# Kernel optimization log

Measured on AMD Instinct MI355X. Metric: run time of the kernel, lower is better.

The kernel has to match this reference:

```python
import math
import jax, jax.numpy as jnp
import numpy as np


def _precompute_psi(nlat_in, nlon_in, nlat_out, K, theta_cutoff):
    """Faithful numpy port of _precompute_convolution_tensor (equiangular grids).
    Returns COO indices (k, t, lat_in, lon_in) and float values of the sparse
    filter tensor psi of logical shape [K, nlat_out, nlat_in*nlon_in]."""
    lats_in = np.linspace(0.0, np.pi, nlat_in)
    lats_out = np.linspace(0.0, np.pi, nlat_out)
    phis = np.linspace(-np.pi, np.pi, nlon_in)
    d_theta = theta_cutoff / K
    theta_i = np.arange(K) * d_theta  # (K,)
    ks, ts, las, los, vs = [], [], [], [], []
    alpha = -lats_in[:, None]          # (nlat_in, 1)
    beta = phis[None, :]               # (1, nlon_in)
    for t in range(nlat_out):
        gamma = lats_out[t]
        z = np.cos(alpha) * np.cos(gamma) - np.cos(beta) * np.sin(alpha) * np.sin(gamma)
        theta = np.arccos(np.clip(z, -1.0, 1.0))   # (nlat_in, nlon_in)
        diff = np.abs(theta[None, :, :] - theta_i[:, None, None])  # (K, nlat_in, nlon_in)
        mask = (diff < d_theta) & (theta[None, :, :] < theta_cutoff)
        k_idx, la_idx, lo_idx = np.nonzero(mask)
        v = 1.0 - diff[k_idx, la_idx, lo_idx] / d_theta  # triangle (hat) weights
        ks.append(k_idx); ts.append(np.full_like(k_idx, t)); las.append(la_idx); los.append(lo_idx); vs.append(v)
    return (np.concatenate(ks).astype(np.int32),
            np.concatenate(ts).astype(np.int32),
            np.concatenate(las).astype(np.int32),
            np.concatenate(los).astype(np.int32),
            np.concatenate(vs).astype(np.float32))


def setup_inputs() -> dict:
    B, C = 4, 32
    nlat_in, nlon_in = 361, 720
    nlat_out, nlon_out = 361, 720
    K = 3
    theta_cutoff = 0.01 * math.pi  # default used at the precompute call site
    k, t, la, lo, v = _precompute_psi(nlat_in, nlon_in, nlat_out, K, theta_cutoff)
    key = jax.random.key(0)
    x = jax.random.normal(key, (B, C, nlat_in, nlon_in), dtype=jnp.float32)
    return {
        "x": x,
        "psi_vals": jnp.asarray(v),
        "psi_k": jnp.asarray(k),
        "psi_t": jnp.asarray(t),
        "psi_lat": jnp.asarray(la),
        "psi_lon": jnp.asarray(lo),
        "kernel_size": K,
        "nlat_out": nlat_out,
        "nlon_out": nlon_out,
    }


def reference(x, psi_vals, psi_k, psi_t, psi_lat, psi_lon, kernel_size, nlat_out, nlon_out):
    B, C, nlat_in, nlon_in = x.shape
    BC = B * C
    scale = nlon_in // nlon_out  # = 1 here
    # (nlat_in, nlon_in, BC) layout, matching x.reshape(B*C,...).permute(1,2,0)
    xr = x.reshape(BC, nlat_in, nlon_in).transpose(1, 2, 0)
    seg = psi_k * nlat_out + psi_t           # row id in the (K*nlat_out) output
    num_seg = kernel_size * nlat_out

    def step(_, p):
        # torch.roll(x, scale, dims=lon) applied (p+1) times before the bmm:
        # rolled[lat, lon] = x[lat, (lon - (p+1)*scale) % nlon]
        lon_idx = (psi_lon - (p + 1) * scale) % nlon_in
        g = xr[psi_lat, lon_idx]             # (nnz, BC) irregular gather
        out_p = jax.ops.segment_sum(psi_vals[:, None] * g, seg, num_segments=num_seg)
        return None, out_p                   # (K*nlat_out, BC)

    _, outs = jax.lax.scan(step, None, jnp.arange(nlon_out))  # (nlon_out, K*nlat_out, BC)
    outs = outs.reshape(nlon_out, kernel_size, nlat_out, BC)
    # permute(3,1,2,0) then split BC -> (B, C)
    return outs.transpose(3, 1, 2, 0).reshape(B, C, kernel_size, nlat_out, nlon_out)
```

## Files before the change

### kernel.cpp

```cpp
#include <hip/hip_runtime.h>
#include <math.h>


#define NLAT 361
#define NLON 720
#define KK 3
#define PTILE 48
#define NPX 15
#define NT 384
#define PD 56
#define SWN 832
#define TOTCAP (720*1024)

typedef __attribute__((ext_vector_type(8))) short bf16x8;
typedef __attribute__((ext_vector_type(4))) float f32x4;
typedef __attribute__((ext_vector_type(4))) unsigned int u32x4;

#define D_PI 3.14159265358979311599796346854418516159057617187500
#define STEP_LAT (D_PI / 360.0)
#define STEP_PHI ((2.0 * D_PI) / 719.0)
#define CUTOFF (0.01 * D_PI)
#define DTH (CUTOFF / 3.0)

__device__ __forceinline__ void gll16(const void* g, void* l) {
    __builtin_amdgcn_global_load_lds(
        (const __attribute__((address_space(1))) void*)g,
        (__attribute__((address_space(3))) void*)l, 16, 0, 0);
}
__device__ __forceinline__ void gll4(const void* g, void* l) {
    __builtin_amdgcn_global_load_lds(
        (const __attribute__((address_space(1))) void*)g,
        (__attribute__((address_space(3))) void*)l, 4, 0, 0);
}

__device__ inline unsigned int bf16pair_rne(float lo, float hi) {
    unsigned int a = __builtin_bit_cast(unsigned int, lo);
    unsigned int b = __builtin_bit_cast(unsigned int, hi);
    a = a + 0x7fffu + ((a >> 16) & 1u);
    b = b + 0x7fffu + ((b >> 16) & 1u);
    return (a >> 16) | (b & 0xffff0000u);
}

__global__ __launch_bounds__(512) void bounds_kernel(int4* __restrict__ params,
                                                     float2* __restrict__ pAB,
                                                     unsigned long long* __restrict__ actd) {
    __shared__ int part[512];
    int tid = threadIdx.x;
    int rmins[9], Ws[9], bl8s[9];
    float As[9], Bs[9];
    int wsum = 0;
    if (tid < NLAT) {
        int t = tid;
        double g = (t == 360) ? D_PI : (double)t * STEP_LAT;
        double cg = cos(g), sg = sin(g);
        const double coscut = cos(CUTOFF);
#pragma unroll
        for (int d = 0; d < 9; ++d) {
            int la = t + d - 4;
            int rmin = 0, W = 0;
            double A = 0.0, Bc = 0.0;
            if (la >= 0 && la <= 360) {
                double lad = (la == 360) ? D_PI : (double)la * STEP_LAT;
                A = cos(lad) * cg;
                Bc = sin(lad) * sg;
                if (Bc < 1e-14) {
                    if (A > coscut) { rmin = 0; W = 720; }
                } else {
                    double C = (coscut - A) / Bc;
                    if (C <= -1.0) { rmin = 0; W = 720; }
                    else if (C < 1.0) {
                        double bmax = acos(C);
                        int r0 = (int)floor((D_PI - bmax) / STEP_PHI) + 1;
                        int r1 = (int)ceil((D_PI + bmax) / STEP_PHI) - 1;
                        if (r0 < 0) r0 = 0;
                        if (r1 > 719) r1 = 719;
                        rmin = r0; W = r1 - r0 + 1;
                        if (W < 0) W = 0;
                    }
                }
            }
            rmins[d] = rmin; Ws[d] = W;
            As[d] = (float)A; Bs[d] = (float)Bc;
            int b8 = 0;
            if (W > 0) {
                b8 = (W + 111) & ~7;
                if (b8 > SWN) b8 = SWN;
            }
            bl8s[d] = b8;
            wsum += b8;
        }
    }
    part[tid] = wsum;
    __syncthreads();
    for (int dd = 1; dd < 512; dd <<= 1) {
        int v = part[tid];
        int w2 = (tid >= dd) ? part[tid - dd] : 0;
        __syncthreads();
        part[tid] = v + w2;
        __syncthreads();
    }
    int base = part[tid] - wsum;
    if (tid < NLAT) {
        unsigned long long pk = 0;
        int nact = 0;
#pragma unroll
        for (int d = 0; d < 9; ++d) {
            int off = base;
            base += bl8s[d];
            if (Ws[d] > 0 && off + bl8s[d] <= TOTCAP) {
                params[tid * 9 + d] = make_int4(rmins[d], Ws[d], off, bl8s[d]);
                pAB[tid * 9 + d] = make_float2(As[d], Bs[d]);
                pk |= ((unsigned long long)d) << (4 + 4 * nact);
                nact++;
            } else {
                params[tid * 9 + d] = make_int4(0, 0, 0, 0);
            }
        }
        pk |= (unsigned long long)nact;
        actd[tid] = pk;
    }
}

__global__ __launch_bounds__(256) void fill_cvt_kernel(const int4* __restrict__ params,
                                                       const float2* __restrict__ pAB,
                                                       unsigned int* __restrict__ wtab,
                                                       const float* __restrict__ x,
                                                       unsigned int* __restrict__ xb,
                                                       int n8, int do_cvt) {
    int bid = blockIdx.x;
    if (bid < NLAT * 9) {
        int4 pr = params[bid];
        int W = pr.y;
        if (W <= 0) return;
        int rmin = pr.x, off = pr.z, bl8 = pr.w;
        float2 ab = pAB[bid];
        float A = ab.x, Bc = ab.y;
        const float invd = (float)(1.0 / DTH);
        for (int idx = threadIdx.x; idx < bl8; idx += 256) {
            int j = idx - PD;
            float f1 = 1.0e9f, f2 = 1.0e9f;
            if (j >= 0 && j < W) {
                int lo = rmin + j;
                float beta = (lo == 719) ? (float)D_PI : (float)((double)lo * STEP_PHI - D_PI);
                float z = fminf(1.f, fmaxf(-1.f, fmaf(Bc, cosf(beta), A)));
                f1 = acosf(z) * invd;
            }
            if (j + 1 >= 0 && j + 1 < W) {
                int lo = rmin + j + 1;
                float beta = (lo == 719) ? (float)D_PI : (float)((double)lo * STEP_PHI - D_PI);
                float z = fminf(1.f, fmaxf(-1.f, fmaf(Bc, cosf(beta), A)));
                f2 = acosf(z) * invd;
            }
            float w0a = fmaxf(0.f, 1.f - f1);
            float w1a = fmaxf(0.f, 1.f - fabsf(f1 - 1.f));
            float w2a = fmaxf(0.f, 1.f - fabsf(f1 - 2.f));
            float w0b = fmaxf(0.f, 1.f - f2);
            float w1b = fmaxf(0.f, 1.f - fabsf(f2 - 1.f));
            float w2b = fmaxf(0.f, 1.f - fabsf(f2 - 2.f));
            wtab[0 * TOTCAP + off + idx] = bf16pair_rne(w0a, w0b);
            wtab[1 * TOTCAP + off + idx] = bf16pair_rne(w1a, w1b);
            wtab[2 * TOTCAP + off + idx] = bf16pair_rne(w2a, w2b);
        }
    } else if (do_cvt) {
        int cb = bid - NLAT * 9;
        for (int i = cb * 256 + threadIdx.x; i < n8; i += 2048 * 256) {
            f32x4 a = *(const f32x4*)(x + (size_t)i * 8);
            f32x4 b = *(const f32x4*)(x + (size_t)i * 8 + 4);
            u32x4 q;
            q.x = bf16pair_rne(a.x, a.y);
            q.y = bf16pair_rne(a.z, a.w);
            q.z = bf16pair_rne(b.x, b.y);
            q.w = bf16pair_rne(b.z, b.w);
            *(u32x4*)(xb + (size_t)i * 4) = q;
        }
    }
}

template <int USEBF16>
__global__ __launch_bounds__(NT, 4) void dconv_mfma_kernel(
    const float* __restrict__ x, const unsigned short* __restrict__ xb,
    const int4* __restrict__ params, const unsigned long long* __restrict__ actd,
    const unsigned int* __restrict__ wtab, float* __restrict__ out) {
    __shared__ __attribute__((aligned(16))) unsigned char sB[2][128 * 128];
    __shared__ unsigned int sWi[2][KK * SWN];

    int bid = blockIdx.x;
    int r = bid & 7;
    int rest = bid >> 3;
    int px = rest % NPX;
    int q = rest / NPX;
    int yp = 8 * q + r;
    if (yp > 360) return;
    int t = (yp & 1) ? (360 - (yp >> 1)) : (yp >> 1);
    int p0 = px * PTILE;
    int tid = threadIdx.x;
    int lane = tid & 63;
    int w = tid >> 6;
    int psub = w >> 1;
    int bc0w = (w & 1) * 64;
    int l15 = lane & 15;
    int l4 = lane >> 4;

    f32x4 acc[4][KK];
#pragma unroll
    for (int n = 0; n < 4; ++n)
#pragma unroll
        for (int k = 0; k < KK; ++k) acc[n][k] = (f32x4){0.f, 0.f, 0.f, 0.f};

    unsigned long long pk = actd[t];
    int nact = (int)(pk & 15ull);

    int c = 0, iact = 0;
    int la = 0, W = 0, off = 0, bl8 = 0, mbase = 0, shift = 0;
    int nK = 0, nC = 1, ks_lo = 0, ks_hi = -1;

    auto LOADP = [&](int dd) {
        la = t + dd - 4;
        int4 pr = params[t * 9 + dd];
        int rmin = pr.x;
        W = pr.y; off = pr.z; bl8 = pr.w;
        int ms0 = rmin - 48 - p0;
        shift = (ms0 + 720) & 7;
        nK = (W + 47 + shift + 31) >> 5;
        nC = (nK + 1) >> 1;
        mbase = (((ms0 - shift) % 720) + 720) % 720;
        int s_off = psub * 16 + 9 - shift;
        int kl = (9 - s_off + 31) >> 5;
        ks_lo = kl < 0 ? 0 : kl;
        int kh = (55 + W - s_off) >> 5;
        ks_hi = kh > nK - 1 ? nK - 1 : kh;
    };

    auto ISSUE = [&](int cc, bool rowstart, int pbuf, int rbuf) {
#pragma unroll
        for (int pass = 0; pass < 3; ++pass) {
            int slot = pass * NT + tid;
            if (slot < 1024) {
                int bc = slot >> 3;
                int g = slot & 7;
                int gs = g ^ (bc & 7);
                int mg = mbase + cc * 64 + gs * 8;
                mg -= (mg >= 720) ? 720 : 0;
                mg -= (mg >= 720) ? 720 : 0;
                mg -= (mg >= 720) ? 720 : 0;
                if (USEBF16) {
                    gll16(xb + ((size_t)bc * NLAT + la) * NLON + mg,
                          &sB[pbuf][slot * 16]);
                } else {
                    const float* src = x + ((size_t)bc * NLAT + la) * NLON + mg;
                    f32x4 a = *(const f32x4*)(src);
                    f32x4 b = *(const f32x4*)(src + 4);
                    u32x4 qq;
                    qq.x = bf16pair_rne(a.x, a.y);
                    qq.y = bf16pair_rne(a.z, a.w);
                    qq.z = bf16pair_rne(b.x, b.y);
                    qq.w = bf16pair_rne(b.z, b.w);
                    *(u32x4*)(&sB[pbuf][slot * 16]) = qq;
                }
            }
        }
        if (rowstart) {
#pragma unroll
            for (int pass = 0; pass < 3; ++pass) {
                int idx = pass * NT + tid;
                if (idx < bl8) {
                    if (USEBF16) {
                        gll4(wtab + 0 * TOTCAP + off + idx, &sWi[rbuf][0 * SWN + idx]);
                        gll4(wtab + 1 * TOTCAP + off + idx, &sWi[rbuf][1 * SWN + idx]);
                        gll4(wtab + 2 * TOTCAP + off + idx, &sWi[rbuf][2 * SWN + idx]);
                    } else {
                        sWi[rbuf][0 * SWN + idx] = wtab[0 * TOTCAP + off + idx];
                        sWi[rbuf][1 * SWN + idx] = wtab[1 * TOTCAP + off + idx];
                        sWi[rbuf][2 * SWN + idx] = wtab[2 * TOTCAP + off + idx];
                    }
                }
            }
        }
    };

    LOADP((int)((pk >> 4) & 15ull));
    ISSUE(0, true, 0, 0);
    int pb = 0, rw = 0;

    while (true) {
        int shiftS = shift;
        int c2 = c * 2;
        int kloS = ks_lo > c2 ? ks_lo : c2;
        int khiS = ks_hi < c2 + 1 ? ks_hi : c2 + 1;
        int pbC = pb, rwC = rw;
        bool done = false, nrow = false;
        if (c + 1 < nC) {
            c = c + 1;
        } else if (iact + 1 < nact) {
            iact++;
            c = 0;
            LOADP((int)((pk >> (4 + 4 * iact)) & 15ull));
            nrow = true;
        } else {
            done = true;
        }
        if (USEBF16) asm volatile("s_waitcnt vmcnt(0)" ::: "memory");
        __syncthreads();
        if (!done) {
            pb ^= 1;
            if (nrow) rw ^= 1;
            ISSUE(c, nrow, pb, rw);
        }
        __builtin_amdgcn_s_setprio(1);
        int soffS = psub * 16 + 9 - shiftS;
        for (int ks = kloS; ks <= khiS; ++ks) {
            int ksl = ks - c2;
            int s = ks * 32 + l4 * 8 + soffS + l15;
            bf16x8 af[KK];
#pragma unroll
            for (int k = 0; k < KK; ++k) {
                const unsigned int* wp = &sWi[rwC][k * SWN + s];
                u32x4 qf;
                qf.x = wp[0];
                qf.y = wp[2];
                qf.z = wp[4];
                qf.w = wp[6];
                af[k] = __builtin_bit_cast(bf16x8, qf);
            }
            int colbase = ksl * 64 + l4 * 16;
#pragma unroll
            for (int n = 0; n < 4; ++n) {
                int brow = bc0w + n * 16 + l15;
                int colb = colbase ^ ((brow & 7) << 4);
                bf16x8 bfv = *(const bf16x8*)(&sB[pbC][brow * 128 + colb]);
                acc[n][0] = __builtin_amdgcn_mfma_f32_16x16x32_bf16(af[0], bfv, acc[n][0], 0, 0, 0);
                acc[n][1] = __builtin_amdgcn_mfma_f32_16x16x32_bf16(af[1], bfv, acc[n][1], 0, 0, 0);
                acc[n][2] = __builtin_amdgcn_mfma_f32_16x16x32_bf16(af[2], bfv, acc[n][2], 0, 0, 0);
            }
        }
        __builtin_amdgcn_s_setprio(0);
        if (done) break;
    }

    int p = p0 + psub * 16 + l4 * 4;
#pragma unroll
    for (int n = 0; n < 4; ++n) {
        int bc = bc0w + n * 16 + l15;
#pragma unroll
        for (int k = 0; k < KK; ++k) {
            float* o = out + (((size_t)bc * KK + k) * NLAT + t) * NLON + p;
            *(f32x4*)o = acc[n][k];
        }
    }
}

extern "C" void kernel_launch(void* const* d_in, const int* in_sizes, int n_in,
                              void* d_out, int out_size, void* d_ws, size_t ws_size,
                              hipStream_t stream) {
    const float* x = (const float*)d_in[0];
    float* out = (float*)d_out;

    char* ws = (char*)d_ws;
    int4* params = (int4*)(ws + 0);
    float2* pAB = (float2*)(ws + 53248);
    unsigned long long* actd = (unsigned long long*)(ws + 81920);
    unsigned int* wtab = (unsigned int*)(ws + 90112);
    size_t xb_off = (90112 + (size_t)3 * TOTCAP * 4 + 4095) & ~(size_t)4095;
    size_t xb_bytes = (size_t)128 * NLAT * NLON * 2;
    int use_bf16 = (ws_size >= xb_off + xb_bytes) ? 1 : 0;
    unsigned short* xb = (unsigned short*)(ws + xb_off);

    int n8 = 128 * NLAT * NLON / 8;

    bounds_kernel<<<1, 512, 0, stream>>>(params, pAB, actd);
    fill_cvt_kernel<<<NLAT * 9 + 2048, 256, 0, stream>>>(params, pAB, wtab, x,
                                                         (unsigned int*)xb, n8, use_bf16);

    dim3 grid(8 * NPX * 46, 1, 1);
    if (use_bf16) {
        dconv_mfma_kernel<1><<<grid, NT, 0, stream>>>(x, xb, params, actd, wtab, out);
    } else {
        dconv_mfma_kernel<0><<<grid, NT, 0, stream>>>(x, xb, params, actd, wtab, out);
    }
}
```

Before: 287.6 us.

## Repack weight window per chunk into contiguous quads for vector LDS reads

```diff
diff --git a/kernel.cpp b/kernel.cpp
--- a/kernel.cpp
+++ b/kernel.cpp
@@ -10,6 +10,7 @@
 #define NT 384
 #define PD 56
 #define SWN 832
+#define SWNP_Q 128
 #define TOTCAP (720*1024)
 
 typedef __attribute__((ext_vector_type(8))) short bf16x8;
@@ -182,7 +183,7 @@
     const int4* __restrict__ params, const unsigned long long* __restrict__ actd,
     const unsigned int* __restrict__ wtab, float* __restrict__ out) {
     __shared__ __attribute__((aligned(16))) unsigned char sB[2][128 * 128];
-    __shared__ unsigned int sWi[2][KK * SWN];
+    __shared__ __attribute__((aligned(16))) unsigned int sWi[2][KK * SWNP_Q * 4];
 
     int bid = blockIdx.x;
     int r = bid & 7;
@@ -231,7 +232,7 @@
         ks_hi = kh > nK - 1 ? nK - 1 : kh;
     };
 
-    auto ISSUE = [&](int cc, bool rowstart, int pbuf, int rbuf) {
+    auto ISSUE = [&](int cc, int pbuf) {
 #pragma unroll
         for (int pass = 0; pass < 3; ++pass) {
             int slot = pass * NT + tid;
@@ -259,43 +260,43 @@
                 }
             }
         }
-        if (rowstart) {
-#pragma unroll
-            for (int pass = 0; pass < 3; ++pass) {
-                int idx = pass * NT + tid;
-                if (idx < bl8) {
-                    if (USEBF16) {
-                        gll4(wtab + 0 * TOTCAP + off + idx, &sWi[rbuf][0 * SWN + idx]);
-                        gll4(wtab + 1 * TOTCAP + off + idx, &sWi[rbuf][1 * SWN + idx]);
-                        gll4(wtab + 2 * TOTCAP + off + idx, &sWi[rbuf][2 * SWN + idx]);
-                    } else {
-                        sWi[rbuf][0 * SWN + idx] = wtab[0 * TOTCAP + off + idx];
-                        sWi[rbuf][1 * SWN + idx] = wtab[1 * TOTCAP + off + idx];
-                        sWi[rbuf][2 * SWN + idx] = wtab[2 * TOTCAP + off + idx];
-                    }
+        int W0 = cc * 64 + 9 - shift;
+        int gmax = off + bl8 - 1;
+#pragma unroll
+        for (int pass = 0; pass < 4; ++pass) {
+            int i = pass * NT + tid;
+            if (i < KK * SWNP_Q * 4) {
+                int plane = i >> 9;
+                int rem = i & 511;
+                int e = rem >> 2;
+                int qq = rem & 3;
+                int gidx = off + W0 + e + 2 * qq;
+                gidx = (gidx > gmax) ? gmax : gidx;
+                if (USEBF16) {
+                    gll4(wtab + (size_t)plane * TOTCAP + gidx, &sWi[pbuf][i]);
+                } else {
+                    sWi[pbuf][i] = wtab[(size_t)plane * TOTCAP + gidx];
                 }
             }
         }
     };
 
     LOADP((int)((pk >> 4) & 15ull));
-    ISSUE(0, true, 0, 0);
-    int pb = 0, rw = 0;
+    ISSUE(0, 0);
+    int pb = 0;
 
     while (true) {
-        int shiftS = shift;
         int c2 = c * 2;
         int kloS = ks_lo > c2 ? ks_lo : c2;
         int khiS = ks_hi < c2 + 1 ? ks_hi : c2 + 1;
-        int pbC = pb, rwC = rw;
-        bool done = false, nrow = false;
+        int pbC = pb;
+        bool done = false;
         if (c + 1 < nC) {
             c = c + 1;
         } else if (iact + 1 < nact) {
             iact++;
             c = 0;
             LOADP((int)((pk >> (4 + 4 * iact)) & 15ull));
-            nrow = true;
         } else {
             done = true;
         }
@@ -303,24 +304,16 @@
         __syncthreads();
         if (!done) {
             pb ^= 1;
-            if (nrow) rw ^= 1;
-            ISSUE(c, nrow, pb, rw);
+            ISSUE(c, pb);
         }
         __builtin_amdgcn_s_setprio(1);
-        int soffS = psub * 16 + 9 - shiftS;
         for (int ks = kloS; ks <= khiS; ++ks) {
             int ksl = ks - c2;
-            int s = ks * 32 + l4 * 8 + soffS + l15;
+            int e = ksl * 32 + l4 * 8 + psub * 16 + l15;
             bf16x8 af[KK];
 #pragma unroll
             for (int k = 0; k < KK; ++k) {
-                const unsigned int* wp = &sWi[rwC][k * SWN + s];
-                u32x4 qf;
-                qf.x = wp[0];
-                qf.y = wp[2];
-                qf.z = wp[4];
-                qf.w = wp[6];
-                af[k] = __builtin_bit_cast(bf16x8, qf);
+                af[k] = *(const bf16x8*)(&sWi[pbC][(k * SWNP_Q + e) * 4]);
             }
             int colbase = ksl * 64 + l4 * 16;
 #pragma unroll
```

After: 308.0 us. 7.1% more time.

## Split wide latitude rows into sub-row segments to shrink weight LDS buffer

Applied to the files above, without the earlier changes.

```diff
diff --git a/kernel.cpp b/kernel.cpp
--- a/kernel.cpp
+++ b/kernel.cpp
@@ -10,7 +10,8 @@
 #define NT 384
 #define PD 56
 #define SWN 832
-#define TOTCAP (720*1024)
+#define SWNL 336
+#define TOTCAP (576*1024)
 
 typedef __attribute__((ext_vector_type(8))) short bf16x8;
 typedef __attribute__((ext_vector_type(4))) float f32x4;
@@ -43,7 +44,8 @@
 
 __global__ __launch_bounds__(512) void bounds_kernel(int4* __restrict__ params,
                                                      float2* __restrict__ pAB,
-                                                     unsigned long long* __restrict__ actd) {
+                                                     unsigned long long* __restrict__ actd,
+                                                     int4* __restrict__ pex) {
     __shared__ int part[512];
     int tid = threadIdx.x;
     int rmins[9], Ws[9], bl8s[9];
@@ -101,8 +103,7 @@
     }
     int base = part[tid] - wsum;
     if (tid < NLAT) {
-        unsigned long long pk = 0;
-        int nact = 0;
+        int cnt = 0;
 #pragma unroll
         for (int d = 0; d < 9; ++d) {
             int off = base;
@@ -110,14 +111,20 @@
             if (Ws[d] > 0 && off + bl8s[d] <= TOTCAP) {
                 params[tid * 9 + d] = make_int4(rmins[d], Ws[d], off, bl8s[d]);
                 pAB[tid * 9 + d] = make_float2(As[d], Bs[d]);
-                pk |= ((unsigned long long)d) << (4 + 4 * nact);
-                nact++;
+                int la = tid + d - 4;
+                int nKmax = (Ws[d] + 85) >> 5;
+                for (int a = 0; a < nKmax; a += 8) {
+                    if (cnt < 32) {
+                        pex[tid * 32 + cnt] =
+                            make_int4(la | (a << 16), Ws[d], rmins[d], off);
+                        cnt++;
+                    }
+                }
             } else {
                 params[tid * 9 + d] = make_int4(0, 0, 0, 0);
             }
         }
-        pk |= (unsigned long long)nact;
-        actd[tid] = pk;
+        actd[tid] = (unsigned long long)cnt;
     }
 }
 
@@ -179,10 +186,10 @@
 template <int USEBF16>
 __global__ __launch_bounds__(NT, 4) void dconv_mfma_kernel(
     const float* __restrict__ x, const unsigned short* __restrict__ xb,
-    const int4* __restrict__ params, const unsigned long long* __restrict__ actd,
+    const int4* __restrict__ pex, const unsigned long long* __restrict__ actd,
     const unsigned int* __restrict__ wtab, float* __restrict__ out) {
     __shared__ __attribute__((aligned(16))) unsigned char sB[2][128 * 128];
-    __shared__ unsigned int sWi[2][KK * SWN];
+    __shared__ unsigned int sWi[2][KK * SWNL];
 
     int bid = blockIdx.x;
     int r = bid & 7;
@@ -207,28 +214,42 @@
 #pragma unroll
         for (int k = 0; k < KK; ++k) acc[n][k] = (f32x4){0.f, 0.f, 0.f, 0.f};
 
-    unsigned long long pk = actd[t];
-    int nact = (int)(pk & 15ull);
+    int nact = (int)actd[t];
 
     int c = 0, iact = 0;
-    int la = 0, W = 0, off = 0, bl8 = 0, mbase = 0, shift = 0;
-    int nK = 0, nC = 1, ks_lo = 0, ks_hi = -1;
-
-    auto LOADP = [&](int dd) {
-        la = t + dd - 4;
-        int4 pr = params[t * 9 + dd];
-        int rmin = pr.x;
-        W = pr.y; off = pr.z; bl8 = pr.w;
+    int la = 0, W = 0, offsub = 0, gmax = 0, mbase = 0, shift = 0, asub = 0;
+    int nC = 1, ks_lo = 0, ks_hi = -1;
+
+    auto LOADP = [&](int i) {
+        int4 pr = pex[t * 32 + i];
+        la = pr.x & 0xFFFF;
+        asub = pr.x >> 16;
+        W = pr.y;
+        int rmin = pr.z;
+        int offrow = pr.w;
         int ms0 = rmin - 48 - p0;
         shift = (ms0 + 720) & 7;
-        nK = (W + 47 + shift + 31) >> 5;
-        nC = (nK + 1) >> 1;
-        mbase = (((ms0 - shift) % 720) + 720) % 720;
+        int nKg = (W + 47 + shift + 31) >> 5;
+        int mb = (((ms0 - shift) % 720) + 720) % 720;
+        mbase = mb + asub * 32;
+        mbase -= (mbase >= 720) ? 720 : 0;
+        mbase -= (mbase >= 720) ? 720 : 0;
+        offsub = offrow + asub * 32;
+        int bl8 = (W + 111) & ~7;
+        if (bl8 > SWN) bl8 = SWN;
+        gmax = offrow + bl8 - 1;
+        int nKp = nKg - asub;
+        if (nKp > 8) nKp = 8;
+        nC = (nKp <= 0) ? 1 : ((nKp + 1) >> 1);
         int s_off = psub * 16 + 9 - shift;
         int kl = (9 - s_off + 31) >> 5;
-        ks_lo = kl < 0 ? 0 : kl;
+        if (kl < 0) kl = 0;
+        if (kl < asub) kl = asub;
+        ks_lo = kl;
         int kh = (55 + W - s_off) >> 5;
-        ks_hi = kh > nK - 1 ? nK - 1 : kh;
+        if (kh > nKg - 1) kh = nKg - 1;
+        if (kh > asub + nKp - 1) kh = asub + nKp - 1;
+        ks_hi = kh;
     };
 
     auto ISSUE = [&](int cc, bool rowstart, int pbuf, int rbuf) {
@@ -262,31 +283,32 @@
         if (rowstart) {
 #pragma unroll
             for (int pass = 0; pass < 3; ++pass) {
-                int idx = pass * NT + tid;
-                if (idx < bl8) {
+                int i = pass * NT + tid;
+                if (i < KK * SWNL) {
+                    int plane = (i >= 2 * SWNL) ? 2 : ((i >= SWNL) ? 1 : 0);
+                    int e = i - plane * SWNL;
+                    int gidx = offsub + e;
+                    gidx = (gidx > gmax) ? gmax : gidx;
                     if (USEBF16) {
-                        gll4(wtab + 0 * TOTCAP + off + idx, &sWi[rbuf][0 * SWN + idx]);
-                        gll4(wtab + 1 * TOTCAP + off + idx, &sWi[rbuf][1 * SWN + idx]);
-                        gll4(wtab + 2 * TOTCAP + off + idx, &sWi[rbuf][2 * SWN + idx]);
+                        gll4(wtab + (size_t)plane * TOTCAP + gidx, &sWi[rbuf][i]);
                     } else {
-                        sWi[rbuf][0 * SWN + idx] = wtab[0 * TOTCAP + off + idx];
-                        sWi[rbuf][1 * SWN + idx] = wtab[1 * TOTCAP + off + idx];
-                        sWi[rbuf][2 * SWN + idx] = wtab[2 * TOTCAP + off + idx];
+                        sWi[rbuf][i] = wtab[(size_t)plane * TOTCAP + gidx];
                     }
                 }
             }
         }
     };
 
-    LOADP((int)((pk >> 4) & 15ull));
+    LOADP(0);
     ISSUE(0, true, 0, 0);
     int pb = 0, rw = 0;
 
     while (true) {
         int shiftS = shift;
-        int c2 = c * 2;
-        int kloS = ks_lo > c2 ? ks_lo : c2;
-        int khiS = ks_hi < c2 + 1 ? ks_hi : c2 + 1;
+        int aS = asub;
+        int base_ks = asub + c * 2;
+        int kloS = ks_lo > base_ks ? ks_lo : base_ks;
+        int khiS = ks_hi < base_ks + 1 ? ks_hi : base_ks + 1;
         int pbC = pb, rwC = rw;
         bool done = false, nrow = false;
         if (c + 1 < nC) {
@@ -294,7 +316,7 @@
         } else if (iact + 1 < nact) {
             iact++;
             c = 0;
-            LOADP((int)((pk >> (4 + 4 * iact)) & 15ull));
+            LOADP(iact);
             nrow = true;
         } else {
             done = true;
@@ -309,12 +331,12 @@
         __builtin_amdgcn_s_setprio(1);
         int soffS = psub * 16 + 9 - shiftS;
         for (int ks = kloS; ks <= khiS; ++ks) {
-            int ksl = ks - c2;
-            int s = ks * 32 + l4 * 8 + soffS + l15;
+            int ksl = ks - base_ks;
+            int sl = (ks - aS) * 32 + l4 * 8 + soffS + l15;
             bf16x8 af[KK];
 #pragma unroll
             for (int k = 0; k < KK; ++k) {
-                const unsigned int* wp = &sWi[rwC][k * SWN + s];
+                const unsigned int* wp = &sWi[rwC][k * SWNL + sl];
                 u32x4 qf;
                 qf.x = wp[0];
                 qf.y = wp[2];
@@ -359,22 +381,23 @@
     int4* params = (int4*)(ws + 0);
     float2* pAB = (float2*)(ws + 53248);
     unsigned long long* actd = (unsigned long long*)(ws + 81920);
-    unsigned int* wtab = (unsigned int*)(ws + 90112);
-    size_t xb_off = (90112 + (size_t)3 * TOTCAP * 4 + 4095) & ~(size_t)4095;
+    int4* pex = (int4*)(ws + 90112);
+    unsigned int* wtab = (unsigned int*)(ws + 278528);
+    size_t xb_off = (278528 + (size_t)3 * TOTCAP * 4 + 4095) & ~(size_t)4095;
     size_t xb_bytes = (size_t)128 * NLAT * NLON * 2;
     int use_bf16 = (ws_size >= xb_off + xb_bytes) ? 1 : 0;
     unsigned short* xb = (unsigned short*)(ws + xb_off);
 
     int n8 = 128 * NLAT * NLON / 8;
 
-    bounds_kernel<<<1, 512, 0, stream>>>(params, pAB, actd);
+    bounds_kernel<<<1, 512, 0, stream>>>(params, pAB, actd, pex);
     fill_cvt_kernel<<<NLAT * 9 + 2048, 256, 0, stream>>>(params, pAB, wtab, x,
                                                          (unsigned int*)xb, n8, use_bf16);
 
     dim3 grid(8 * NPX * 46, 1, 1);
     if (use_bf16) {
-        dconv_mfma_kernel<1><<<grid, NT, 0, stream>>>(x, xb, params, actd, wtab, out);
+        dconv_mfma_kernel<1><<<grid, NT, 0, stream>>>(x, xb, pex, actd, wtab, out);
     } else {
-        dconv_mfma_kernel<0><<<grid, NT, 0, stream>>>(x, xb, params, actd, wtab, out);
-    }
-}
+        dconv_mfma_kernel<0><<<grid, NT, 0, stream>>>(x, xb, pex, actd, wtab, out);
+    }
+}
```

After: 301.7 us. 1.05x slower.
